# Kernel tuning notes

Measured on AMD Instinct MI355X. Metric: run time of the kernel, lower is better.

## Reference

```python
import jax, jax.numpy as jnp
import numpy as np


def _conv1x1(x, W, b):
    # 1x1 conv == per-pixel channel matmul: x [B,C,H,W], W [O,C], b [O]
    return jnp.einsum('bchw,oc->bohw', x, W) + b[None, :, None, None]


def setup_inputs() -> dict:
    key = jax.random.key(0)
    ks = jax.random.split(key, 9)
    B, C, H, W = 16, 512, 32, 32
    s = 1.0 / np.sqrt(C)
    inp = {
        'x': jax.random.normal(ks[0], (B, C, H, W), dtype=jnp.float32),
        'Wq': jax.random.normal(ks[1], (C, C), dtype=jnp.float32) * s,
        'bq': jax.random.normal(ks[2], (C,), dtype=jnp.float32) * 0.01,
        'Wk': jax.random.normal(ks[3], (C, C), dtype=jnp.float32) * s,
        'bk': jax.random.normal(ks[4], (C,), dtype=jnp.float32) * 0.01,
        'Wv': jax.random.normal(ks[5], (C, C), dtype=jnp.float32) * s,
        'bv': jax.random.normal(ks[6], (C,), dtype=jnp.float32) * 0.01,
        'Wo': jax.random.normal(ks[7], (C, C), dtype=jnp.float32) * s,
        'bo': jax.random.normal(ks[8], (C,), dtype=jnp.float32) * 0.01,
    }
    return inp


def reference(x, Wq, bq, Wk, bk, Wv, bv, Wo, bo):
    B, C, H, W = x.shape
    q = _conv1x1(x, Wq, bq)
    k = _conv1x1(x, Wk, bk)
    v = _conv1x1(x, Wv, bv)
    hw = H * W
    qf = q.reshape(B, C, hw)  # [B,C,HW]
    kf = k.reshape(B, C, hw)
    vf = v.reshape(B, C, hw)
    # scores[b,i,j] = sum_c q[b,c,i] * k[b,c,j], scaled by c^-0.5
    scores = jnp.einsum('bci,bcj->bij', qf, kf) * (C ** -0.5)
    attn = jax.nn.softmax(scores, axis=2)  # softmax over keys j
    # out[b,c,i] = sum_j v[b,c,j] * attn[b,i,j]
    out = jnp.einsum('bcj,bij->bci', vf, attn).reshape(B, C, H, W)
    out = _conv1x1(out, Wo, bo)
    return x + out
```

## Files before the change

### kernel.cpp

```cpp
#include <hip/hip_runtime.h>
#include <hip/hip_bf16.h>
#include <math.h>


typedef __bf16 bf16x8 __attribute__((ext_vector_type(8)));
typedef float  f32x4  __attribute__((ext_vector_type(4)));

__device__ __forceinline__ unsigned short f2bf(float f) {
    unsigned u = __float_as_uint(f);
    u += 0x7fff + ((u >> 16) & 1);
    return (unsigned short)(u >> 16);
}

__device__ __forceinline__ void gload_lds16(const void* g, void* l) {
    __builtin_amdgcn_global_load_lds(
        (const __attribute__((address_space(1))) void*)g,
        (__attribute__((address_space(3))) void*)l, 16, 0, 0);
}

template<bool OUT_F32, int BIAS_MODE, bool RESID, int EXPM>
__global__ __launch_bounds__(256) void gemm_bt_mfma(
    const unsigned short* __restrict__ A, const unsigned short* __restrict__ B,
    void* __restrict__ Cout, const float* __restrict__ bias,
    const float* __restrict__ resid, float* __restrict__ lsum,
    int M, int N, int K, int ldA, int ldB,
    long sA, long sB, long sC, long sR, float scale)
{
    __shared__ unsigned short Als[128 * 32];
    __shared__ unsigned short Bls[128 * 32];

    const int bz = blockIdx.z;
    A += bz * sA;
    B += bz * sB;
    const int m0 = blockIdx.y * 128;
    const int n0 = blockIdx.x * 128;

    const int tid  = threadIdx.x;
    const int lane = tid & 63;
    const int wave = tid >> 6;
    const int wm   = wave >> 1;
    const int wn   = wave & 1;

    const int ar = lane >> 2;
    const int ak = (lane & 3) * 8;

    const unsigned short* agp0 = A + (long)(m0 + wave * 16 + ar) * ldA + ak;
    const unsigned short* agp1 = agp0 + 64L * ldA;
    const unsigned short* bgp0 = B + (long)(n0 + wave * 16 + ar) * ldB + ak;
    const unsigned short* bgp1 = bgp0 + 64L * ldB;
    unsigned short* al0 = Als + wave * 512;
    unsigned short* al1 = Als + (wave + 4) * 512;
    unsigned short* bl0 = Bls + wave * 512;
    unsigned short* bl1 = Bls + (wave + 4) * 512;

    const int fr = lane & 15;
    const int fq = lane >> 4;

    f32x4 acc[4][4] = {};

    for (int k0 = 0; k0 < K; k0 += 32) {
        gload_lds16(agp0, al0);
        gload_lds16(agp1, al1);
        gload_lds16(bgp0, bl0);
        gload_lds16(bgp1, bl1);
        agp0 += 32; agp1 += 32; bgp0 += 32; bgp1 += 32;
        __syncthreads();

        bf16x8 af[4], bfr[4];
        #pragma unroll
        for (int mt = 0; mt < 4; ++mt)
            af[mt] = *(const bf16x8*)&Als[(wm * 64 + mt * 16 + fr) * 32 + fq * 8];
        #pragma unroll
        for (int nt = 0; nt < 4; ++nt)
            bfr[nt] = *(const bf16x8*)&Bls[(wn * 64 + nt * 16 + fr) * 32 + fq * 8];

        #pragma unroll
        for (int mt = 0; mt < 4; ++mt)
            #pragma unroll
            for (int nt = 0; nt < 4; ++nt)
                acc[mt][nt] = __builtin_amdgcn_mfma_f32_16x16x32_bf16(
                    af[mt], bfr[nt], acc[mt][nt], 0, 0, 0);
        __syncthreads();
    }

    float* Cf = (float*)Cout + bz * sC;
    unsigned short* Ch = (unsigned short*)Cout + bz * sC;
    if (RESID) resid += bz * sR;

    if (EXPM == 1) {
        float* lrow = lsum + bz * (long)M;
        #pragma unroll
        for (int mt = 0; mt < 4; ++mt) {
            const int row = m0 + wm * 64 + mt * 16 + fq * 4;
            #pragma unroll
            for (int r = 0; r < 4; ++r) {
                float rs = 0.0f;
                #pragma unroll
                for (int nt = 0; nt < 4; ++nt) {
                    const int col = n0 + wn * 64 + nt * 16 + fr;
                    const float e = __expf(acc[mt][nt][r] * scale);
                    rs += e;
                    Ch[(long)(row + r) * N + col] = f2bf(e);
                }
                rs += __shfl_xor(rs, 1);
                rs += __shfl_xor(rs, 2);
                rs += __shfl_xor(rs, 4);
                rs += __shfl_xor(rs, 8);
                if (fr == 0) atomicAdd(&lrow[row + r], rs);
            }
        }
    } else {
        float linv[4][4];
        if (EXPM == 2) {
            const float* lrow = lsum + bz * (long)M;
            #pragma unroll
            for (int mt = 0; mt < 4; ++mt)
                #pragma unroll
                for (int r = 0; r < 4; ++r)
                    linv[mt][r] = 1.0f / lrow[m0 + wm * 64 + mt * 16 + fq * 4 + r];
        }
        #pragma unroll
        for (int nt = 0; nt < 4; ++nt) {
            const int col = n0 + wn * 64 + nt * 16 + fr;
            const float bn = (BIAS_MODE == 2) ? bias[col] : 0.0f;
            #pragma unroll
            for (int mt = 0; mt < 4; ++mt) {
                const int row = m0 + wm * 64 + mt * 16 + fq * 4;
                #pragma unroll
                for (int r = 0; r < 4; ++r) {
                    float val = acc[mt][nt][r] + bn;
                    if (BIAS_MODE == 1) val += bias[row + r];
                    if (EXPM == 2) val *= linv[mt][r];
                    const long idx = (long)(row + r) * N + col;
                    if (RESID) val += resid[idx];
                    if (OUT_F32) Cf[idx] = val;
                    else         Ch[idx] = f2bf(val);
                }
            }
        }
    }
}

__global__ __launch_bounds__(256) void transpose_cast(
    const float* __restrict__ x, unsigned short* __restrict__ xT)
{
    __shared__ float t[32][33];
    const int b = blockIdx.z;
    const int p0 = blockIdx.x * 32;
    const int c0 = blockIdx.y * 32;
    const float* xb = x + (long)b * 524288;
    unsigned short* xTb = xT + (long)b * 524288;
    const int tx = threadIdx.x & 31;
    const int ty = threadIdx.x >> 5;
    #pragma unroll
    for (int i = 0; i < 4; ++i)
        t[ty + 8 * i][tx] = xb[(long)(c0 + ty + 8 * i) * 1024 + p0 + tx];
    __syncthreads();
    #pragma unroll
    for (int i = 0; i < 4; ++i)
        xTb[(long)(p0 + ty + 8 * i) * 512 + c0 + tx] = f2bf(t[tx][ty + 8 * i]);
}

__global__ __launch_bounds__(256) void prep(
    const float* __restrict__ Wq, const float* __restrict__ Wk,
    const float* __restrict__ Wv, const float* __restrict__ Wo,
    const float* __restrict__ bq, const float* __restrict__ bk,
    unsigned short* __restrict__ Wb, float* __restrict__ biasqk,
    float* __restrict__ lsum)
{
    const int b = blockIdx.x;
    const int t = threadIdx.x;
    if (b < 1024) {
        const float* srcs[4] = {Wq, Wk, Wv, Wo};
        const float* s = srcs[b >> 8];
        unsigned short* d = Wb + (long)(b >> 8) * 262144;
        const int i = ((b & 255) * 256 + t) * 4;
        const float4 f = *(const float4*)(s + i);
        ushort4 h;
        h.x = f2bf(f.x); h.y = f2bf(f.y); h.z = f2bf(f.z); h.w = f2bf(f.w);
        *(ushort4*)(d + i) = h;
    } else {
        biasqk[t]       = bq[t];
        biasqk[256 + t] = bq[256 + t];
        biasqk[512 + t] = bk[t];
        biasqk[768 + t] = bk[256 + t];
        #pragma unroll
        for (int i = 0; i < 64; ++i) lsum[i * 256 + t] = 0.0f;
    }
}

extern "C" void kernel_launch(void* const* d_in, const int* in_sizes, int n_in,
                              void* d_out, int out_size, void* d_ws, size_t ws_size,
                              hipStream_t stream)
{
    const float* x  = (const float*)d_in[0];
    const float* Wq = (const float*)d_in[1];
    const float* bq = (const float*)d_in[2];
    const float* Wk = (const float*)d_in[3];
    const float* bk = (const float*)d_in[4];
    const float* Wv = (const float*)d_in[5];
    const float* bv = (const float*)d_in[6];
    const float* Wo = (const float*)d_in[7];
    const float* bo = (const float*)d_in[8];
    float* out = (float*)d_out;

    const int Bn = 16, C = 512, HW = 1024;
    const long CHW = (long)C * HW;
    const long SHW = (long)HW * HW;

    unsigned short* xT   = (unsigned short*)d_ws;
    unsigned short* qkT  = xT + Bn * CHW;
    unsigned short* vB   = qkT + Bn * SHW;
    unsigned short* expS = vB + Bn * CHW;
    unsigned short* Wb   = expS + Bn * SHW;
    float* biasqk = (float*)(Wb + 4 * 262144);
    float* lsum   = biasqk + 1024;
    unsigned short* OT = xT;

    unsigned short* Wvb = Wb + 2 * 262144;
    unsigned short* Wob = Wb + 3 * 262144;

    const dim3 blk(256);
    const float scale = 0.044194173824159216f;

    prep<<<dim3(1025), blk, 0, stream>>>(Wq, Wk, Wv, Wo, bq, bk, Wb, biasqk, lsum);
    transpose_cast<<<dim3(32, 16, Bn), blk, 0, stream>>>(x, xT);

    gemm_bt_mfma<false, 2, false, 0><<<dim3(8, 8, Bn), blk, 0, stream>>>(
        xT, Wb, qkT, biasqk, nullptr, nullptr,
        HW, 2 * C, C, C, C, CHW, 0, SHW, 0, 0.0f);

    gemm_bt_mfma<false, 1, false, 0><<<dim3(8, 4, Bn), blk, 0, stream>>>(
        Wvb, xT, vB, bv, nullptr, nullptr,
        C, HW, C, C, C, 0, CHW, CHW, 0, 0.0f);

    gemm_bt_mfma<false, 0, false, 1><<<dim3(8, 8, Bn), blk, 0, stream>>>(
        qkT, qkT + C, expS, nullptr, nullptr, lsum,
        HW, HW, C, 2 * C, 2 * C, SHW, SHW, SHW, 0, scale);

    gemm_bt_mfma<false, 0, false, 2><<<dim3(4, 8, Bn), blk, 0, stream>>>(
        expS, vB, OT, nullptr, nullptr, lsum,
        HW, C, HW, HW, HW, SHW, CHW, CHW, 0, 0.0f);

    gemm_bt_mfma<true, 1, true, 0><<<dim3(8, 4, Bn), blk, 0, stream>>>(
        Wob, OT, out, bo, x, nullptr,
        C, HW, C, C, C, 0, CHW, CHW, CHW, 0.0f);
}
```

Measured before the change: 248.9 us.

## Remap GEMM blocks per XCD, deepen K step to 64, fuse prep kernels

The GEMM kernel now uses a 1D grid and maps block IDs so that each XCD (blockIdx mod 8) handles two whole batches. This is meant to improve L2 locality of the shared A/B operands. The K loop now loads 64 columns per iteration into two LDS halves, halving the number of barriers per tile at the cost of double the LDS footprint. The transpose/cast and weight-prep kernels are merged into one launch to remove a kernel launch boundary.

```diff
diff --git a/kernel.cpp b/kernel.cpp
--- a/kernel.cpp
+++ b/kernel.cpp
@@ -24,16 +24,22 @@
     void* __restrict__ Cout, const float* __restrict__ bias,
     const float* __restrict__ resid, float* __restrict__ lsum,
     int M, int N, int K, int ldA, int ldB,
-    long sA, long sB, long sC, long sR, float scale)
+    long sA, long sB, long sC, long sR,
+    int ln_nn, int ln_pb, float scale)
 {
-    __shared__ unsigned short Als[128 * 32];
-    __shared__ unsigned short Bls[128 * 32];
-
-    const int bz = blockIdx.z;
+    __shared__ unsigned short Als[2][128 * 32];
+    __shared__ unsigned short Bls[2][128 * 32];
+
+    const int L   = blockIdx.x;
+    const int xcd = L & 7;
+    const int idx = L >> 3;
+    const int bz  = xcd * 2 + (idx >> ln_pb);
+    const int w   = idx & ((1 << ln_pb) - 1);
+    const int m0  = (w >> ln_nn) << 7;
+    const int n0  = (w & ((1 << ln_nn) - 1)) << 7;
+
     A += bz * sA;
     B += bz * sB;
-    const int m0 = blockIdx.y * 128;
-    const int n0 = blockIdx.x * 128;
 
     const int tid  = threadIdx.x;
     const int lane = tid & 63;
@@ -44,42 +50,53 @@
     const int ar = lane >> 2;
     const int ak = (lane & 3) * 8;
 
-    const unsigned short* agp0 = A + (long)(m0 + wave * 16 + ar) * ldA + ak;
-    const unsigned short* agp1 = agp0 + 64L * ldA;
-    const unsigned short* bgp0 = B + (long)(n0 + wave * 16 + ar) * ldB + ak;
-    const unsigned short* bgp1 = bgp0 + 64L * ldB;
-    unsigned short* al0 = Als + wave * 512;
-    unsigned short* al1 = Als + (wave + 4) * 512;
-    unsigned short* bl0 = Bls + wave * 512;
-    unsigned short* bl1 = Bls + (wave + 4) * 512;
+    const unsigned short* agp = A + (long)(m0 + wave * 16 + ar) * ldA + ak;
+    const unsigned short* bgp = B + (long)(n0 + wave * 16 + ar) * ldB + ak;
+    const long aj = 64L * ldA;
+    const long bj = 64L * ldB;
+    unsigned short* al0 = Als[0] + wave * 512;
+    unsigned short* al0h = Als[0] + (wave + 4) * 512;
+    unsigned short* al1 = Als[1] + wave * 512;
+    unsigned short* al1h = Als[1] + (wave + 4) * 512;
+    unsigned short* bl0 = Bls[0] + wave * 512;
+    unsigned short* bl0h = Bls[0] + (wave + 4) * 512;
+    unsigned short* bl1 = Bls[1] + wave * 512;
+    unsigned short* bl1h = Bls[1] + (wave + 4) * 512;
 
     const int fr = lane & 15;
     const int fq = lane >> 4;
 
     f32x4 acc[4][4] = {};
 
-    for (int k0 = 0; k0 < K; k0 += 32) {
-        gload_lds16(agp0, al0);
-        gload_lds16(agp1, al1);
-        gload_lds16(bgp0, bl0);
-        gload_lds16(bgp1, bl1);
-        agp0 += 32; agp1 += 32; bgp0 += 32; bgp1 += 32;
+    for (int k0 = 0; k0 < K; k0 += 64) {
+        gload_lds16(agp,           al0);
+        gload_lds16(agp + aj,      al0h);
+        gload_lds16(agp + 32,      al1);
+        gload_lds16(agp + 32 + aj, al1h);
+        gload_lds16(bgp,           bl0);
+        gload_lds16(bgp + bj,      bl0h);
+        gload_lds16(bgp + 32,      bl1);
+        gload_lds16(bgp + 32 + bj, bl1h);
+        agp += 64; bgp += 64;
         __syncthreads();
 
-        bf16x8 af[4], bfr[4];
-        #pragma unroll
-        for (int mt = 0; mt < 4; ++mt)
-            af[mt] = *(const bf16x8*)&Als[(wm * 64 + mt * 16 + fr) * 32 + fq * 8];
-        #pragma unroll
-        for (int nt = 0; nt < 4; ++nt)
-            bfr[nt] = *(const bf16x8*)&Bls[(wn * 64 + nt * 16 + fr) * 32 + fq * 8];
-
-        #pragma unroll
-        for (int mt = 0; mt < 4; ++mt)
+        #pragma unroll
+        for (int p = 0; p < 2; ++p) {
+            bf16x8 af[4], bfr[4];
+            #pragma unroll
+            for (int mt = 0; mt < 4; ++mt)
+                af[mt] = *(const bf16x8*)&Als[p][(wm * 64 + mt * 16 + fr) * 32 + fq * 8];
             #pragma unroll
             for (int nt = 0; nt < 4; ++nt)
-                acc[mt][nt] = __builtin_amdgcn_mfma_f32_16x16x32_bf16(
-                    af[mt], bfr[nt], acc[mt][nt], 0, 0, 0);
+                bfr[nt] = *(const bf16x8*)&Bls[p][(wn * 64 + nt * 16 + fr) * 32 + fq * 8];
+
+            #pragma unroll
+            for (int mt = 0; mt < 4; ++mt)
+                #pragma unroll
+                for (int nt = 0; nt < 4; ++nt)
+                    acc[mt][nt] = __builtin_amdgcn_mfma_f32_16x16x32_bf16(
+                        af[mt], bfr[nt], acc[mt][nt], 0, 0, 0);
+        }
         __syncthreads();
     }
 
@@ -141,27 +158,8 @@
     }
 }
 
-__global__ __launch_bounds__(256) void transpose_cast(
-    const float* __restrict__ x, unsigned short* __restrict__ xT)
-{
-    __shared__ float t[32][33];
-    const int b = blockIdx.z;
-    const int p0 = blockIdx.x * 32;
-    const int c0 = blockIdx.y * 32;
-    const float* xb = x + (long)b * 524288;
-    unsigned short* xTb = xT + (long)b * 524288;
-    const int tx = threadIdx.x & 31;
-    const int ty = threadIdx.x >> 5;
-    #pragma unroll
-    for (int i = 0; i < 4; ++i)
-        t[ty + 8 * i][tx] = xb[(long)(c0 + ty + 8 * i) * 1024 + p0 + tx];
-    __syncthreads();
-    #pragma unroll
-    for (int i = 0; i < 4; ++i)
-        xTb[(long)(p0 + ty + 8 * i) * 512 + c0 + tx] = f2bf(t[tx][ty + 8 * i]);
-}
-
-__global__ __launch_bounds__(256) void prep(
+__global__ __launch_bounds__(256) void prep_all(
+    const float* __restrict__ x, unsigned short* __restrict__ xT,
     const float* __restrict__ Wq, const float* __restrict__ Wk,
     const float* __restrict__ Wv, const float* __restrict__ Wo,
     const float* __restrict__ bq, const float* __restrict__ bk,
@@ -170,11 +168,29 @@
 {
     const int b = blockIdx.x;
     const int t = threadIdx.x;
-    if (b < 1024) {
+    if (b < 8192) {
+        __shared__ float tl[32][33];
+        const int batch = b >> 9;
+        const int rem = b & 511;
+        const int p0 = (rem & 31) * 32;
+        const int c0 = (rem >> 5) * 32;
+        const float* xb = x + (long)batch * 524288;
+        unsigned short* xTb = xT + (long)batch * 524288;
+        const int tx = t & 31;
+        const int ty = t >> 5;
+        #pragma unroll
+        for (int i = 0; i < 4; ++i)
+            tl[ty + 8 * i][tx] = xb[(long)(c0 + ty + 8 * i) * 1024 + p0 + tx];
+        __syncthreads();
+        #pragma unroll
+        for (int i = 0; i < 4; ++i)
+            xTb[(long)(p0 + ty + 8 * i) * 512 + c0 + tx] = f2bf(tl[tx][ty + 8 * i]);
+    } else if (b < 9216) {
+        const int wb = b - 8192;
         const float* srcs[4] = {Wq, Wk, Wv, Wo};
-        const float* s = srcs[b >> 8];
-        unsigned short* d = Wb + (long)(b >> 8) * 262144;
-        const int i = ((b & 255) * 256 + t) * 4;
+        const float* s = srcs[wb >> 8];
+        unsigned short* d = Wb + (long)(wb >> 8) * 262144;
+        const int i = ((wb & 255) * 256 + t) * 4;
         const float4 f = *(const float4*)(s + i);
         ushort4 h;
         h.x = f2bf(f.x); h.y = f2bf(f.y); h.z = f2bf(f.z); h.w = f2bf(f.w);
@@ -223,26 +239,26 @@
     const dim3 blk(256);
     const float scale = 0.044194173824159216f;
 
-    prep<<<dim3(1025), blk, 0, stream>>>(Wq, Wk, Wv, Wo, bq, bk, Wb, biasqk, lsum);
-    transpose_cast<<<dim3(32, 16, Bn), blk, 0, stream>>>(x, xT);
-
-    gemm_bt_mfma<false, 2, false, 0><<<dim3(8, 8, Bn), blk, 0, stream>>>(
+    prep_all<<<dim3(9217), blk, 0, stream>>>(x, xT, Wq, Wk, Wv, Wo, bq, bk,
+                                             Wb, biasqk, lsum);
+
+    gemm_bt_mfma<false, 2, false, 0><<<dim3(1024), blk, 0, stream>>>(
         xT, Wb, qkT, biasqk, nullptr, nullptr,
-        HW, 2 * C, C, C, C, CHW, 0, SHW, 0, 0.0f);
-
-    gemm_bt_mfma<false, 1, false, 0><<<dim3(8, 4, Bn), blk, 0, stream>>>(
+        HW, 2 * C, C, C, C, CHW, 0, SHW, 0, 3, 6, 0.0f);
+
+    gemm_bt_mfma<false, 1, false, 0><<<dim3(512), blk, 0, stream>>>(
         Wvb, xT, vB, bv, nullptr, nullptr,
-        C, HW, C, C, C, 0, CHW, CHW, 0, 0.0f);
-
-    gemm_bt_mfma<false, 0, false, 1><<<dim3(8, 8, Bn), blk, 0, stream>>>(
+        C, HW, C, C, C, 0, CHW, CHW, 0, 3, 5, 0.0f);
+
+    gemm_bt_mfma<false, 0, false, 1><<<dim3(1024), blk, 0, stream>>>(
         qkT, qkT + C, expS, nullptr, nullptr, lsum,
-        HW, HW, C, 2 * C, 2 * C, SHW, SHW, SHW, 0, scale);
-
-    gemm_bt_mfma<false, 0, false, 2><<<dim3(4, 8, Bn), blk, 0, stream>>>(
+        HW, HW, C, 2 * C, 2 * C, SHW, SHW, SHW, 0, 3, 6, scale);
+
+    gemm_bt_mfma<false, 0, false, 2><<<dim3(512), blk, 0, stream>>>(
         expS, vB, OT, nullptr, nullptr, lsum,
-        HW, C, HW, HW, HW, SHW, CHW, CHW, 0, 0.0f);
-
-    gemm_bt_mfma<true, 1, true, 0><<<dim3(8, 4, Bn), blk, 0, stream>>>(
+        HW, C, HW, HW, HW, SHW, CHW, CHW, 0, 2, 5, 0.0f);
+
+    gemm_bt_mfma<true, 1, true, 0><<<dim3(512), blk, 0, stream>>>(
         Wob, OT, out, bo, x, nullptr,
-        C, HW, C, C, C, 0, CHW, CHW, CHW, 0.0f);
-}
+        C, HW, C, C, C, 0, CHW, CHW, CHW, 3, 5, 0.0f);
+}
```

Result: faster. 217.6 us (-12.6%).
